# Optimization experiments

Measured on AMD Instinct MI355X. Metric: run time of the kernel, lower is better.

## Reference

```python
import jax, jax.numpy as jnp
import numpy as np
from jax import lax

B, CIN, COUT, H, W, K, PAD = 8, 64, 64, 256, 256, 3, 1

def setup_inputs() -> dict:
    key = jax.random.key(0)
    k1, k2, k3, k4 = jax.random.split(key, 4)
    x = jax.random.normal(k1, (B, CIN, H, W), dtype=jnp.float32)
    mask = (jax.random.uniform(k2, (B, 1, H, W)) < 0.5).astype(jnp.float32)
    fan_in = CIN * K * K
    bound = 1.0 / np.sqrt(fan_in)
    weight = jax.random.uniform(k3, (COUT, CIN, K, K), minval=-bound, maxval=bound, dtype=jnp.float32)
    bias = jax.random.uniform(k4, (COUT,), minval=-bound, maxval=bound, dtype=jnp.float32)
    return {"x": x, "mask": mask, "weight": weight, "bias": bias}

def _masked_conv(x, mask, weight, bias):
    # Standard conv: the original gathers valid unfold columns, matmuls with the
    # flattened weight + bias, and scatters back; zeros elsewhere. Equivalent to
    # (conv(x) + b) * valid, where valid[b,l] = any(mask patch at l != 0).
    conv = lax.conv_general_dilated(
        x, weight,
        window_strides=(1, 1),
        padding=[(PAD, PAD), (PAD, PAD)],
        dimension_numbers=("NCHW", "OIHW", "NCHW"),
    )
    out = conv + bias[None, :, None, None]
    # any(|mask| != 0) over each KxK window == max-pool of |mask| > 0
    pooled = lax.reduce_window(
        jnp.abs(mask), 0.0, lax.max,
        window_dimensions=(1, 1, K, K),
        window_strides=(1, 1, 1, 1),
        padding=[(0, 0), (0, 0), (PAD, PAD), (PAD, PAD)],
    )
    valid = pooled > 0  # [B,1,H,W], broadcasts over channels
    return jnp.where(valid, out, jnp.zeros((), dtype=out.dtype))

def reference(x, mask, weight, bias):
    return _masked_conv(x, mask, weight, bias)
```

## Files before the change

kernel.cpp:

```cpp
#include <hip/hip_runtime.h>


#define B_    8
#define C_    64
#define H_    256
#define W_    256
#define HW_   (H_ * W_)

typedef __attribute__((ext_vector_type(8))) short bf16x8;
typedef __attribute__((ext_vector_type(4))) float f32x4;

__device__ __forceinline__ unsigned short f2bf(float f) {
    unsigned int u = __float_as_uint(f);
    u = (u + 0x7FFFu + ((u >> 16) & 1u)) >> 16;
    return (unsigned short)u;
}

__global__ __launch_bounds__(256) void wconv(const float* __restrict__ wgt,
                                             unsigned short* __restrict__ wsA)
{
    const int gid  = blockIdx.x * 256 + threadIdx.x;
    const int s    = gid >> 8;
    const int rest = gid & 255;
    const int mf   = rest >> 6;
    const int lane = rest & 63;
    const int tap  = s >> 1;
    const int kblk = s & 1;
    const int kh = tap / 3, kw = tap % 3;
    const int co = mf * 16 + (lane & 15);
    unsigned short v[8];
#pragma unroll
    for (int j = 0; j < 8; ++j) {
        const int ci = kblk * 32 + (lane >> 4) * 8 + j;
        v[j] = f2bf(wgt[((co * C_ + ci) * 3 + kh) * 3 + kw]);
    }
    unsigned short* dst = wsA + (size_t)gid * 8;
    *(uint4*)dst = *(const uint4*)v;
}

#define TROWS 6
#define TCOLS 34
#define NU    (TROWS * TCOLS * 8)
#define NCHUNK 4
#define NTAIL (NU - 3 * 512)

__global__ __launch_bounds__(512, 6) void masked_conv_mfma(
    const float* __restrict__ x,
    const float* __restrict__ mask,
    const unsigned short* __restrict__ wsA,
    const float* __restrict__ bias,
    float* __restrict__ out)
{
    __shared__ __align__(16) unsigned short xs[TROWS * TCOLS * 64];

    const int tid  = threadIdx.x;
    const int wave = tid >> 6;
    const int lane = tid & 63;
    const int l15  = lane & 15;
    const int lq   = lane >> 4;

    const int w0 = blockIdx.x * 32;
    const int h0 = blockIdx.y * 4;
    const int b  = blockIdx.z;

    const float* xb = x + (size_t)b * C_ * HW_;

    const int hrow = wave & 3;
    const int ch   = wave >> 2;
    const int h    = h0 + hrow;
    const int pcol = w0 + (lane & 31);

    int valid = 0;
    {
        const float* mb = mask + (size_t)b * HW_;
#pragma unroll
        for (int dh = -1; dh <= 1; ++dh) {
#pragma unroll
            for (int dw = -1; dw <= 1; ++dw) {
                const int hh = h + dh;
                const int ww = pcol + dw;
                const int ok = (hh >= 0) & (hh < H_) & (ww >= 0) & (ww < W_);
                const float mv = mb[ok ? (hh * W_ + ww) : 0];
                valid |= ok & (mv != 0.0f ? 1 : 0);
            }
        }
    }

    float va[NCHUNK][8];
    int   cell[NCHUNK];
    int   okf[NCHUNK];
#pragma unroll
    for (int k = 0; k < NCHUNK; ++k) {
        const int u0 = tid + (k << 9);
        const int u  = (u0 < NU) ? u0 : 0;
        const int col = u % TCOLS;
        const int t2  = u / TCOLS;
        const int oct = t2 & 7;
        const int row = t2 >> 3;
        const int gh = h0 - 1 + row;
        const int gw = w0 - 1 + col;
        const int ok = (gh >= 0) & (gh < H_) & (gw >= 0) & (gw < W_);
        const float* px = xb + ((size_t)(oct * 8) * H_ + (ok ? gh : 0)) * W_
                             + (ok ? gw : 0);
#pragma unroll
        for (int j = 0; j < 8; ++j) va[k][j] = px[(size_t)j * HW_];
        const int c = row * TCOLS + col;
        cell[k] = (c << 6) + ((oct ^ (c & 7)) << 3);
        okf[k]  = ok;
    }
#pragma unroll
    for (int k = 0; k < NCHUNK; ++k) {
        if (k == NCHUNK - 1 && tid >= NTAIL) continue;
        unsigned short v[8];
#pragma unroll
        for (int j = 0; j < 8; ++j)
            v[j] = okf[k] ? f2bf(va[k][j]) : (unsigned short)0;
        *(uint4*)&xs[cell[k]] = *(const uint4*)v;
    }

    __syncthreads();

    const int vn0 = __builtin_amdgcn_ds_bpermute(l15 << 2, valid);
    const int vn1 = __builtin_amdgcn_ds_bpermute((16 + l15) << 2, valid);

    f32x4 acc[2][2];
#pragma unroll
    for (int mf = 0; mf < 2; ++mf)
#pragma unroll
        for (int nf = 0; nf < 2; ++nf)
            acc[mf][nf] = (f32x4){0.f, 0.f, 0.f, 0.f};

    const bf16x8* wA = (const bf16x8*)wsA;

#pragma unroll 1
    for (int kh = 0; kh < 3; ++kh) {
        const int rowbase = (hrow + kh) * TCOLS;
#pragma unroll
        for (int kw = 0; kw < 3; ++kw) {
#pragma unroll
            for (int kblk = 0; kblk < 2; ++kblk) {
                const int s = (kh * 3 + kw) * 2 + kblk;
                bf16x8 a[2];
#pragma unroll
                for (int mf = 0; mf < 2; ++mf)
                    a[mf] = wA[(s * 4 + ch * 2 + mf) * 64 + lane];
                bf16x8 bfv[2];
#pragma unroll
                for (int nf = 0; nf < 2; ++nf) {
                    const int cell2 = rowbase + nf * 16 + l15 + kw;
                    const int g = kblk * 4 + lq;
                    bfv[nf] = *(const bf16x8*)
                        &xs[(cell2 << 6) + ((g ^ (cell2 & 7)) << 3)];
                }
#pragma unroll
                for (int mf = 0; mf < 2; ++mf)
#pragma unroll
                    for (int nf = 0; nf < 2; ++nf)
                        acc[mf][nf] = __builtin_amdgcn_mfma_f32_16x16x32_bf16(
                            a[mf], bfv[nf], acc[mf][nf], 0, 0, 0);
            }
        }
    }

#pragma unroll
    for (int nf = 0; nf < 2; ++nf) {
        const int cloc = nf * 16 + l15;
        const int vn = nf ? vn1 : vn0;
        float* ob = out + ((size_t)(b * C_) * H_ + h) * W_ + w0 + cloc;
#pragma unroll
        for (int mf = 0; mf < 2; ++mf) {
#pragma unroll
            for (int reg = 0; reg < 4; ++reg) {
                const int co = ch * 32 + mf * 16 + lq * 4 + reg;
                const float val = vn ? (acc[mf][nf][reg] + bias[co]) : 0.0f;
                ob[(size_t)co * HW_] = val;
            }
        }
    }
}

extern "C" void kernel_launch(void* const* d_in, const int* in_sizes, int n_in,
                              void* d_out, int out_size, void* d_ws, size_t ws_size,
                              hipStream_t stream) {
    const float* x    = (const float*)d_in[0];
    const float* mask = (const float*)d_in[1];
    const float* wgt  = (const float*)d_in[2];
    const float* bias = (const float*)d_in[3];
    float* out        = (float*)d_out;
    unsigned short* wsA = (unsigned short*)d_ws;

    wconv<<<18, 256, 0, stream>>>(wgt, wsA);

    dim3 grid(W_ / 32, H_ / 4, B_);
    masked_conv_mfma<<<grid, 512, 0, stream>>>(x, mask, wsA, bias, out);
}
```

Baseline: 327.5 us.

## Make conv blocks persistent over eight row tiles with double-buffered LDS staging

Each block now processes eight consecutive 4-row tiles instead of one. Global loads for the next tile's input halo are issued before the MFMA loop of the current tile, and written to a second LDS buffer afterward, so load latency overlaps compute. The mask loads are also issued early and reduced after the MMA loop. The grid shrinks eightfold, LDS doubles and launch bounds drop to 4 blocks per CU. This risks lower occupancy and higher register pressure from holding 32 prefetched floats across the compute loop.

```diff
diff --git a/kernel.cpp b/kernel.cpp
--- a/kernel.cpp
+++ b/kernel.cpp
@@ -43,15 +43,17 @@
 #define NU    (TROWS * TCOLS * 8)
 #define NCHUNK 4
 #define NTAIL (NU - 3 * 512)
-
-__global__ __launch_bounds__(512, 6) void masked_conv_mfma(
+#define BUFSZ (TROWS * TCOLS * 64)
+#define TILES 8
+
+__global__ __launch_bounds__(512, 4) void masked_conv_mfma(
     const float* __restrict__ x,
     const float* __restrict__ mask,
     const unsigned short* __restrict__ wsA,
     const float* __restrict__ bias,
     float* __restrict__ out)
 {
-    __shared__ __align__(16) unsigned short xs[TROWS * TCOLS * 64];
+    __shared__ __align__(16) unsigned short xs[2 * BUFSZ];
 
     const int tid  = threadIdx.x;
     const int wave = tid >> 6;
@@ -59,36 +61,18 @@
     const int l15  = lane & 15;
     const int lq   = lane >> 4;
 
-    const int w0 = blockIdx.x * 32;
-    const int h0 = blockIdx.y * 4;
-    const int b  = blockIdx.z;
+    const int w0    = blockIdx.x * 32;
+    const int hbase = blockIdx.y * (4 * TILES);
+    const int b     = blockIdx.z;
 
     const float* xb = x + (size_t)b * C_ * HW_;
+    const float* mb = mask + (size_t)b * HW_;
 
     const int hrow = wave & 3;
     const int ch   = wave >> 2;
-    const int h    = h0 + hrow;
     const int pcol = w0 + (lane & 31);
 
-    int valid = 0;
-    {
-        const float* mb = mask + (size_t)b * HW_;
-#pragma unroll
-        for (int dh = -1; dh <= 1; ++dh) {
-#pragma unroll
-            for (int dw = -1; dw <= 1; ++dw) {
-                const int hh = h + dh;
-                const int ww = pcol + dw;
-                const int ok = (hh >= 0) & (hh < H_) & (ww >= 0) & (ww < W_);
-                const float mv = mb[ok ? (hh * W_ + ww) : 0];
-                valid |= ok & (mv != 0.0f ? 1 : 0);
-            }
-        }
-    }
-
-    float va[NCHUNK][8];
-    int   cell[NCHUNK];
-    int   okf[NCHUNK];
+    int ldsoff[NCHUNK], eoff[NCHUNK], rowk[NCHUNK], okwk[NCHUNK];
 #pragma unroll
     for (int k = 0; k < NCHUNK; ++k) {
         const int u0 = tid + (k << 9);
@@ -97,83 +81,135 @@
         const int t2  = u / TCOLS;
         const int oct = t2 & 7;
         const int row = t2 >> 3;
-        const int gh = h0 - 1 + row;
-        const int gw = w0 - 1 + col;
-        const int ok = (gh >= 0) & (gh < H_) & (gw >= 0) & (gw < W_);
-        const float* px = xb + ((size_t)(oct * 8) * H_ + (ok ? gh : 0)) * W_
-                             + (ok ? gw : 0);
-#pragma unroll
-        for (int j = 0; j < 8; ++j) va[k][j] = px[(size_t)j * HW_];
+        const int gw  = w0 - 1 + col;
+        okwk[k] = (gw >= 0) & (gw < W_);
+        const int gwc = gw < 0 ? 0 : (gw >= W_ ? W_ - 1 : gw);
+        eoff[k] = oct * 8 * HW_ + gwc;
         const int c = row * TCOLS + col;
-        cell[k] = (c << 6) + ((oct ^ (c & 7)) << 3);
-        okf[k]  = ok;
+        ldsoff[k] = (c << 6) + ((oct ^ (c & 7)) << 3);
+        rowk[k] = row;
     }
-#pragma unroll
-    for (int k = 0; k < NCHUNK; ++k) {
-        if (k == NCHUNK - 1 && tid >= NTAIL) continue;
-        unsigned short v[8];
-#pragma unroll
-        for (int j = 0; j < 8; ++j)
-            v[j] = okf[k] ? f2bf(va[k][j]) : (unsigned short)0;
-        *(uint4*)&xs[cell[k]] = *(const uint4*)v;
-    }
-
+
+    float va[NCHUNK][8];
+    int   okf[NCHUNK];
+
+    auto stage_issue = [&](int t) {
+        const int h0 = hbase + 4 * t;
+#pragma unroll
+        for (int k = 0; k < NCHUNK; ++k) {
+            const int gh  = h0 - 1 + rowk[k];
+            const int okh = (gh >= 0) & (gh < H_);
+            const int ghc = gh < 0 ? 0 : (gh >= H_ ? H_ - 1 : gh);
+            okf[k] = okwk[k] & okh;
+            const float* px = xb + eoff[k] + (size_t)ghc * W_;
+#pragma unroll
+            for (int j = 0; j < 8; ++j) va[k][j] = px[(size_t)j * HW_];
+        }
+    };
+    auto stage_write = [&](int bsel) {
+        unsigned short* dst = xs + bsel * BUFSZ;
+#pragma unroll
+        for (int k = 0; k < NCHUNK; ++k) {
+            if (k == NCHUNK - 1 && tid >= NTAIL) continue;
+            unsigned short v[8];
+#pragma unroll
+            for (int j = 0; j < 8; ++j)
+                v[j] = okf[k] ? f2bf(va[k][j]) : (unsigned short)0;
+            *(uint4*)&dst[ldsoff[k]] = *(const uint4*)v;
+        }
+    };
+
+    const bf16x8* wA = (const bf16x8*)wsA;
+
+    stage_issue(0);
+    stage_write(0);
     __syncthreads();
 
-    const int vn0 = __builtin_amdgcn_ds_bpermute(l15 << 2, valid);
-    const int vn1 = __builtin_amdgcn_ds_bpermute((16 + l15) << 2, valid);
-
-    f32x4 acc[2][2];
-#pragma unroll
-    for (int mf = 0; mf < 2; ++mf)
-#pragma unroll
-        for (int nf = 0; nf < 2; ++nf)
-            acc[mf][nf] = (f32x4){0.f, 0.f, 0.f, 0.f};
-
-    const bf16x8* wA = (const bf16x8*)wsA;
-
 #pragma unroll 1
-    for (int kh = 0; kh < 3; ++kh) {
-        const int rowbase = (hrow + kh) * TCOLS;
-#pragma unroll
-        for (int kw = 0; kw < 3; ++kw) {
-#pragma unroll
-            for (int kblk = 0; kblk < 2; ++kblk) {
-                const int s = (kh * 3 + kw) * 2 + kblk;
-                bf16x8 a[2];
-#pragma unroll
-                for (int mf = 0; mf < 2; ++mf)
-                    a[mf] = wA[(s * 4 + ch * 2 + mf) * 64 + lane];
-                bf16x8 bfv[2];
-#pragma unroll
-                for (int nf = 0; nf < 2; ++nf) {
-                    const int cell2 = rowbase + nf * 16 + l15 + kw;
-                    const int g = kblk * 4 + lq;
-                    bfv[nf] = *(const bf16x8*)
-                        &xs[(cell2 << 6) + ((g ^ (cell2 & 7)) << 3)];
+    for (int t = 0; t < TILES; ++t) {
+        const int h = hbase + 4 * t + hrow;
+
+        if (t + 1 < TILES) stage_issue(t + 1);
+
+        float mv[9];
+        int okm = 0;
+        {
+            int i = 0;
+#pragma unroll
+            for (int dh = -1; dh <= 1; ++dh) {
+#pragma unroll
+                for (int dw = -1; dw <= 1; ++dw, ++i) {
+                    const int hh = h + dh;
+                    const int ww = pcol + dw;
+                    const int ok = (hh >= 0) & (hh < H_) & (ww >= 0) & (ww < W_);
+                    mv[i] = mb[ok ? (hh * W_ + ww) : 0];
+                    okm |= ok << i;
                 }
-#pragma unroll
-                for (int mf = 0; mf < 2; ++mf)
-#pragma unroll
-                    for (int nf = 0; nf < 2; ++nf)
-                        acc[mf][nf] = __builtin_amdgcn_mfma_f32_16x16x32_bf16(
-                            a[mf], bfv[nf], acc[mf][nf], 0, 0, 0);
             }
         }
-    }
-
-#pragma unroll
-    for (int nf = 0; nf < 2; ++nf) {
-        const int cloc = nf * 16 + l15;
-        const int vn = nf ? vn1 : vn0;
-        float* ob = out + ((size_t)(b * C_) * H_ + h) * W_ + w0 + cloc;
-#pragma unroll
-        for (int mf = 0; mf < 2; ++mf) {
-#pragma unroll
-            for (int reg = 0; reg < 4; ++reg) {
-                const int co = ch * 32 + mf * 16 + lq * 4 + reg;
-                const float val = vn ? (acc[mf][nf][reg] + bias[co]) : 0.0f;
-                ob[(size_t)co * HW_] = val;
+        __builtin_amdgcn_sched_barrier(0);
+
+        const unsigned short* xbuf = xs + (t & 1) * BUFSZ;
+        f32x4 acc[2][2];
+#pragma unroll
+        for (int mf = 0; mf < 2; ++mf)
+#pragma unroll
+            for (int nf = 0; nf < 2; ++nf)
+                acc[mf][nf] = (f32x4){0.f, 0.f, 0.f, 0.f};
+
+#pragma unroll 1
+        for (int kh = 0; kh < 3; ++kh) {
+            const int rowbase = (hrow + kh) * TCOLS;
+#pragma unroll
+            for (int kw = 0; kw < 3; ++kw) {
+#pragma unroll
+                for (int kblk = 0; kblk < 2; ++kblk) {
+                    const int s = (kh * 3 + kw) * 2 + kblk;
+                    bf16x8 a[2];
+#pragma unroll
+                    for (int mf = 0; mf < 2; ++mf)
+                        a[mf] = wA[(s * 4 + ch * 2 + mf) * 64 + lane];
+                    bf16x8 bfv[2];
+#pragma unroll
+                    for (int nf = 0; nf < 2; ++nf) {
+                        const int cell2 = rowbase + nf * 16 + l15 + kw;
+                        const int g = kblk * 4 + lq;
+                        bfv[nf] = *(const bf16x8*)
+                            &xbuf[(cell2 << 6) + ((g ^ (cell2 & 7)) << 3)];
+                    }
+#pragma unroll
+                    for (int mf = 0; mf < 2; ++mf)
+#pragma unroll
+                        for (int nf = 0; nf < 2; ++nf)
+                            acc[mf][nf] = __builtin_amdgcn_mfma_f32_16x16x32_bf16(
+                                a[mf], bfv[nf], acc[mf][nf], 0, 0, 0);
+                }
+            }
+        }
+
+        int valid = 0;
+#pragma unroll
+        for (int i = 0; i < 9; ++i)
+            valid |= ((okm >> i) & 1) & (mv[i] != 0.0f ? 1 : 0);
+        const int vn0 = __builtin_amdgcn_ds_bpermute(l15 << 2, valid);
+        const int vn1 = __builtin_amdgcn_ds_bpermute((16 + l15) << 2, valid);
+
+        if (t + 1 < TILES) stage_write((t + 1) & 1);
+        __syncthreads();
+
+#pragma unroll
+        for (int nf = 0; nf < 2; ++nf) {
+            const int cloc = nf * 16 + l15;
+            const int vn = nf ? vn1 : vn0;
+            float* ob = out + ((size_t)(b * C_) * H_ + h) * W_ + w0 + cloc;
+#pragma unroll
+            for (int mf = 0; mf < 2; ++mf) {
+#pragma unroll
+                for (int reg = 0; reg < 4; ++reg) {
+                    const int co = ch * 32 + mf * 16 + lq * 4 + reg;
+                    const float val = vn ? (acc[mf][nf][reg] + bias[co]) : 0.0f;
+                    ob[(size_t)co * HW_] = val;
+                }
             }
         }
     }
@@ -191,6 +227,6 @@
 
     wconv<<<18, 256, 0, stream>>>(wgt, wsA);
 
-    dim3 grid(W_ / 32, H_ / 4, B_);
+    dim3 grid(W_ / 32, H_ / (4 * TILES), B_);
     masked_conv_mfma<<<grid, 512, 0, stream>>>(x, mask, wsA, bias, out);
 }
```

Measured after the change: 372.7 us. 13.8% more time.
